# Kernel tuning notes

Measured on AMD Instinct MI355X. Metric: run time of the kernel, lower is better.

Reference implementation:

```python
import jax, jax.numpy as jnp
import numpy as np

N_NODES = 50000
N_EDGES = 600000
D = 128
BN_EPS = 1e-5


def _linear_init(key, fan_in, fan_out):
    # torch nn.Linear default: U(-1/sqrt(fan_in), 1/sqrt(fan_in)) for W and b
    kw, kb = jax.random.split(key)
    bound = 1.0 / np.sqrt(fan_in)
    W = jax.random.uniform(kw, (fan_in, fan_out), minval=-bound, maxval=bound, dtype=jnp.float32)
    b = jax.random.uniform(kb, (fan_out,), minval=-bound, maxval=bound, dtype=jnp.float32)
    return W, b


def setup_inputs() -> dict:
    key = jax.random.key(0)
    ks = jax.random.split(key, 8)
    x = jax.random.normal(ks[0], (N_NODES, D), dtype=jnp.float32)
    edge_index = jax.random.randint(ks[1], (2, N_EDGES), 0, N_NODES, dtype=jnp.int32)
    edge_attr = jax.random.normal(ks[2], (N_EDGES, D), dtype=jnp.float32)
    # MLP: [2D, D, D, D] -> Linear(2D,D)+SiLU+BN, Linear(D,D)+SiLU+BN, Linear(D,D)
    W1, b1 = _linear_init(ks[3], 2 * D, D)
    W2, b2 = _linear_init(ks[4], D, D)
    W3, b3 = _linear_init(ks[5], D, D)
    g1 = jnp.ones((D,), jnp.float32); be1 = jnp.zeros((D,), jnp.float32)
    g2 = jnp.ones((D,), jnp.float32); be2 = jnp.zeros((D,), jnp.float32)
    return {"x": x, "edge_index": edge_index, "edge_attr": edge_attr,
            "W1": W1, "b1": b1, "g1": g1, "be1": be1,
            "W2": W2, "b2": b2, "g2": g2, "be2": be2,
            "W3": W3, "b3": b3}


def _bn(h, gamma, beta):
    # BatchNorm1d in training mode: normalize with batch statistics (biased var)
    mean = jnp.mean(h, axis=0)
    var = jnp.var(h, axis=0)
    return (h - mean) * jax.lax.rsqrt(var + BN_EPS) * gamma + beta


def reference(x, edge_index, edge_attr, W1, b1, g1, be1, W2, b2, g2, be2, W3, b3):
    src = edge_index[0]
    # scatter_add over edges indexed by source node -> [N_NODES, D]
    agg = jax.ops.segment_sum(edge_attr, src, num_segments=x.shape[0])
    h = jnp.concatenate([x, agg], axis=1)  # [N, 2D]
    h = _bn(jax.nn.silu(h @ W1 + b1), g1, be1)
    h = _bn(jax.nn.silu(h @ W2 + b2), g2, be2)
    return h @ W3 + b3
```

## Files before the change

kernel.cpp:

```cpp
#include <hip/hip_runtime.h>
#include <hip/hip_bf16.h>

#define D 128

typedef __attribute__((ext_vector_type(8))) short bfrag;
typedef __attribute__((ext_vector_type(4))) float facc;
typedef __attribute__((ext_vector_type(4))) unsigned int u32x4;

__device__ __forceinline__ facc mfma16(bfrag a, bfrag b, facc c) {
    return __builtin_amdgcn_mfma_f32_16x16x32_bf16(a, b, c, 0, 0, 0);
}
__device__ __forceinline__ unsigned int bf16_rn(float f) {
    unsigned int u = __float_as_uint(f);
    u += 0x7FFF + ((u >> 16) & 1);
    return u >> 16;
}
__device__ __forceinline__ float bf16_f(unsigned int h) {
    return __uint_as_float(h << 16);
}
__device__ __forceinline__ unsigned int packf(float v) {
    unsigned int hi = bf16_rn(v);
    unsigned int lo = bf16_rn(v - bf16_f(hi));
    return (hi << 16) | lo;
}

__global__ void hist_kernel(const int* __restrict__ src,
                            int* __restrict__ counts, int nedges) {
    int e = blockIdx.x * 256 + threadIdx.x;
    if (e < nedges) atomicAdd(&counts[src[e]], 1);
}

__global__ __launch_bounds__(1024) void scan_kernel(
    const int* __restrict__ counts, int* __restrict__ off,
    int* __restrict__ cur, int n) {
    __shared__ int sdata[1024];
    const int tid = threadIdx.x;
    const int per = (n + 1023) / 1024;
    const int lo = min(tid * per, n);
    const int hi = min(lo + per, n);
    int sum = 0;
#pragma unroll 4
    for (int i = lo; i < hi; ++i) sum += counts[i];
    sdata[tid] = sum;
    __syncthreads();
#pragma unroll
    for (int d = 1; d < 1024; d <<= 1) {
        int v = (tid >= d) ? sdata[tid - d] : 0;
        __syncthreads();
        sdata[tid] += v;
        __syncthreads();
    }
    int pre = (tid == 0) ? 0 : sdata[tid - 1];
#pragma unroll 4
    for (int i = lo; i < hi; ++i) {
        off[i] = pre;
        cur[i] = pre;
        pre += counts[i];
    }
    if (tid == 0) off[n] = sdata[1023];
}

__global__ void fill_kernel(const int* __restrict__ src, int* __restrict__ cur,
                            int* __restrict__ eid, int nedges) {
    int e = blockIdx.x * 256 + threadIdx.x;
    if (e < nedges) {
        int slot = atomicAdd(&cur[src[e]], 1);
        eid[slot] = e;
    }
}

__global__ __launch_bounds__(256) void gather_kernel(
    const float* __restrict__ edge_attr, const int* __restrict__ eid,
    const int* __restrict__ off, unsigned int* __restrict__ aggp, int nnodes) {
    int node = blockIdx.x * 4 + (threadIdx.x >> 6);
    int lane = threadIdx.x & 63;
    if (node >= nnodes) return;
    int s = off[node];
    int e = off[node + 1];
    float2 acc = make_float2(0.f, 0.f);
    int i = s;
    for (; i + 8 <= e; i += 8) {
        int eb[8];
#pragma unroll
        for (int u = 0; u < 8; ++u) eb[u] = eid[i + u];
#pragma unroll
        for (int u = 0; u < 8; ++u) {
            float2 v = *((const float2*)(edge_attr + (size_t)eb[u] * D) + lane);
            acc.x += v.x;
            acc.y += v.y;
        }
    }
    for (; i < e; ++i) {
        float2 v = *((const float2*)(edge_attr + (size_t)eid[i] * D) + lane);
        acc.x += v.x;
        acc.y += v.y;
    }
    uint2 p;
    p.x = packf(acc.x);
    p.y = packf(acc.y);
    *((uint2*)(aggp + (size_t)node * D) + lane) = p;
}

__global__ void split_kernel(const float* __restrict__ x,
                             unsigned int* __restrict__ xp, int n4) {
    int i = blockIdx.x * 256 + threadIdx.x;
    if (i < n4) {
        float4 v = ((const float4*)x)[i];
        uint4 p;
        p.x = packf(v.x);
        p.y = packf(v.y);
        p.z = packf(v.z);
        p.w = packf(v.w);
        ((uint4*)xp)[i] = p;
    }
}

__global__ void prep_w_kernel(const float* __restrict__ W,
                              unsigned short* __restrict__ Wh,
                              unsigned short* __restrict__ Wl) {
    int j = blockIdx.x;
    int k = threadIdx.x;
    float w = W[(size_t)k * D + j];
    unsigned int hi = bf16_rn(w);
    size_t o = (size_t)((k >> 3) * 128 + j) * 8 + (k & 7);
    Wh[o] = (unsigned short)hi;
    Wl[o] = (unsigned short)bf16_rn(w - bf16_f(hi));
}

__global__ void fold_kernel(const float* __restrict__ sum,
                            const float* __restrict__ sq,
                            const float* __restrict__ gamma,
                            const float* __restrict__ beta,
                            const float* __restrict__ W,
                            const float* __restrict__ b,
                            unsigned short* __restrict__ Wh,
                            unsigned short* __restrict__ Wl,
                            float* __restrict__ bf, float invM) {
    int j = blockIdx.x;
    int k = threadIdx.x;
    float mean = sum[k] * invM;
    float var = sq[k] * invM - mean * mean;
    float scale = gamma[k] * rsqrtf(var + 1e-5f);
    float shift = beta[k] - mean * scale;
    float w = W[k * D + j];
    float wf = scale * w;
    unsigned int hi = bf16_rn(wf);
    size_t o = (size_t)((k >> 3) * 128 + j) * 8 + (k & 7);
    Wh[o] = (unsigned short)hi;
    Wl[o] = (unsigned short)bf16_rn(wf - bf16_f(hi));
    float v = shift * w;
#pragma unroll
    for (int of = 32; of; of >>= 1) v += __shfl_down(v, of);
    __shared__ float ws2[2];
    if ((k & 63) == 0) ws2[k >> 6] = v;
    __syncthreads();
    if (k == 0) bf[j] = b[j] + ws2[0] + ws2[1];
}

template <int K, bool SILU, bool STATS, bool PACKOUT>
__global__ __launch_bounds__(256, 2) void gemm_mfma(
    const unsigned int* __restrict__ A0, const unsigned int* __restrict__ A1,
    const unsigned short* __restrict__ Wh,
    const unsigned short* __restrict__ Wl,
    const float* __restrict__ bias, unsigned int* __restrict__ Cp,
    float* __restrict__ Cf, float* __restrict__ gsum,
    float* __restrict__ gsq, int M) {
    constexpr int NS = K / 32;
    const int tid = threadIdx.x;
    const int w = tid >> 6;
    const int l = tid & 63;
    const int lr = l & 15;
    const int lk = l >> 4;
    const int row0 = blockIdx.x * 128 + w * 32;

    facc acc[2][8];
#pragma unroll
    for (int rt = 0; rt < 2; ++rt)
#pragma unroll
        for (int ct = 0; ct < 8; ++ct)
#pragma unroll
            for (int r = 0; r < 4; ++r) acc[rt][ct][r] = 0.f;

    for (int s = 0; s < NS; ++s) {
        const int kb = s * 32 + lk * 8;
        bfrag ah[2], al[2];
#pragma unroll
        for (int rt = 0; rt < 2; ++rt) {
            const int arow = row0 + rt * 16 + lr;
            const unsigned int* As = A0;
            int kk = kb;
            if (K == 256 && s >= 4) { As = A1; kk = kb - 128; }
            u32x4 q0 = {0u, 0u, 0u, 0u}, q1 = {0u, 0u, 0u, 0u};
            if (arow < M) {
                const u32x4* p = (const u32x4*)(As + (size_t)arow * D + kk);
                q0 = p[0];
                q1 = p[1];
            }
            unsigned int ua[8] = {q0.x, q0.y, q0.z, q0.w,
                                  q1.x, q1.y, q1.z, q1.w};
            u32x4 uh, ul;
#pragma unroll
            for (int r = 0; r < 4; ++r) {
                uh[r] = __builtin_amdgcn_perm(ua[2 * r + 1], ua[2 * r],
                                              0x07060302u);
                ul[r] = __builtin_amdgcn_perm(ua[2 * r + 1], ua[2 * r],
                                              0x05040100u);
            }
            ah[rt] = __builtin_bit_cast(bfrag, uh);
            al[rt] = __builtin_bit_cast(bfrag, ul);
        }
        bfrag bh[8], bl[8];
        const int fb = (s * 4 + lk) * 128;
#pragma unroll
        for (int ct = 0; ct < 8; ++ct) {
            size_t o = (size_t)(fb + ct * 16 + lr) * 8;
            bh[ct] = *(const bfrag*)(Wh + o);
            bl[ct] = *(const bfrag*)(Wl + o);
        }
#pragma unroll
        for (int rt = 0; rt < 2; ++rt)
#pragma unroll
            for (int ct = 0; ct < 8; ++ct)
                acc[rt][ct] = mfma16(ah[rt], bh[ct], acc[rt][ct]);
#pragma unroll
        for (int rt = 0; rt < 2; ++rt)
#pragma unroll
            for (int ct = 0; ct < 8; ++ct)
                acc[rt][ct] = mfma16(ah[rt], bl[ct], acc[rt][ct]);
#pragma unroll
        for (int rt = 0; rt < 2; ++rt)
#pragma unroll
            for (int ct = 0; ct < 8; ++ct)
                acc[rt][ct] = mfma16(al[rt], bh[ct], acc[rt][ct]);
    }

    __shared__ float sred[2][4][128];
#pragma unroll
    for (int ct = 0; ct < 8; ++ct) {
        const int col = ct * 16 + lr;
        const float bj = bias[col];
        float s = 0.f, q = 0.f;
#pragma unroll
        for (int rt = 0; rt < 2; ++rt) {
            const int base = row0 + rt * 16 + lk * 4;
#pragma unroll
            for (int r = 0; r < 4; ++r) {
                int crow = base + r;
                if (crow < M) {
                    float v = acc[rt][ct][r] + bj;
                    if (SILU) v = v / (1.0f + __expf(-v));
                    if (PACKOUT) Cp[(size_t)crow * D + col] = packf(v);
                    else         Cf[(size_t)crow * D + col] = v;
                    if (STATS) { s += v; q += v * v; }
                }
            }
        }
        if (STATS) {
            s += __shfl_xor(s, 16);
            s += __shfl_xor(s, 32);
            q += __shfl_xor(q, 16);
            q += __shfl_xor(q, 32);
            if (lk == 0) {
                sred[0][w][col] = s;
                sred[1][w][col] = q;
            }
        }
    }
    if (STATS) {
        __syncthreads();
        if (tid < 128) {
            float v = sred[0][0][tid] + sred[0][1][tid] + sred[0][2][tid] +
                      sred[0][3][tid];
            unsafeAtomicAdd(&gsum[tid], v);
        } else {
            int c = tid - 128;
            float v = sred[1][0][c] + sred[1][1][c] + sred[1][2][c] +
                      sred[1][3][c];
            unsafeAtomicAdd(&gsq[c], v);
        }
    }
}

extern "C" void kernel_launch(void* const* d_in, const int* in_sizes, int n_in,
                              void* d_out, int out_size, void* d_ws,
                              size_t ws_size, hipStream_t stream) {
    const float* x     = (const float*)d_in[0];
    const int*   eidx  = (const int*)d_in[1];
    const float* eattr = (const float*)d_in[2];
    const float* W1  = (const float*)d_in[3];
    const float* b1  = (const float*)d_in[4];
    const float* g1  = (const float*)d_in[5];
    const float* be1 = (const float*)d_in[6];
    const float* W2  = (const float*)d_in[7];
    const float* b2  = (const float*)d_in[8];
    const float* g2  = (const float*)d_in[9];
    const float* be2 = (const float*)d_in[10];
    const float* W3  = (const float*)d_in[11];
    const float* b3  = (const float*)d_in[12];

    const int M = in_sizes[0] / D;
    const int E = in_sizes[1] / 2;
    const int* srcIdx = eidx;

    unsigned int* wsu = (unsigned int*)d_ws;
    unsigned int* aggp = wsu;
    unsigned int* xp   = aggp + (size_t)M * D;
    unsigned int* h1p  = xp + (size_t)M * D;
    unsigned int* h2p  = h1p + (size_t)M * D;
    float* sum1 = (float*)(h2p + (size_t)M * D);
    float* sq1  = sum1 + D;
    float* sum2 = sq1 + D;
    float* sq2  = sum2 + D;
    float* b2f  = sq2 + D;
    float* b3f  = b2f + D;
    int* counts = (int*)(b3f + D);
    int* off    = counts + M;
    int* cur    = off + M + 4;
    int* eid    = cur + M;
    unsigned short* W1h = (unsigned short*)(eid + E);
    unsigned short* W1l = W1h + 256 * D;
    unsigned short* W2h = W1l + 256 * D;
    unsigned short* W2l = W2h + D * D;
    unsigned short* W3h = W2l + D * D;
    unsigned short* W3l = W3h + D * D;

    float* out = (float*)d_out;

    hipMemsetAsync(counts, 0, (size_t)M * sizeof(int), stream);
    hipMemsetAsync(sum1, 0, 4 * D * sizeof(float), stream);

    int eblk = (E + 255) / 256;
    hist_kernel<<<eblk, 256, 0, stream>>>(srcIdx, counts, E);
    scan_kernel<<<1, 1024, 0, stream>>>(counts, off, cur, M);
    fill_kernel<<<eblk, 256, 0, stream>>>(srcIdx, cur, eid, E);
    gather_kernel<<<(M + 3) / 4, 256, 0, stream>>>(eattr, eid, off, aggp, M);

    split_kernel<<<(M * 32 + 255) / 256, 256, 0, stream>>>(x, xp, M * 32);
    prep_w_kernel<<<D, 256, 0, stream>>>(W1, W1h, W1l);

    int nblk = (M + 127) / 128;
    gemm_mfma<256, true, true, true><<<nblk, 256, 0, stream>>>(
        xp, aggp, W1h, W1l, b1, h1p, nullptr, sum1, sq1, M);
    fold_kernel<<<D, D, 0, stream>>>(sum1, sq1, g1, be1, W2, b2, W2h, W2l,
                                     b2f, 1.0f / (float)M);
    gemm_mfma<128, true, true, true><<<nblk, 256, 0, stream>>>(
        h1p, nullptr, W2h, W2l, b2f, h2p, nullptr, sum2, sq2, M);
    fold_kernel<<<D, D, 0, stream>>>(sum2, sq2, g2, be2, W3, b3, W3h, W3l,
                                     b3f, 1.0f / (float)M);
    gemm_mfma<128, false, false, false><<<nblk, 256, 0, stream>>>(
        h2p, nullptr, W3h, W3l, b3f, nullptr, out, nullptr, nullptr, M);
}
```

Before: 289.8 us.

## Merge prep kernels, parallelize prefix scan, and vectorize edge gather

Merges the histogram, x bf16 split, and W1 split kernels into one launch using block-index ranges. Replaces the single-block 1024-thread scan with a three-phase multi-block scan so the offset computation is no longer serialized on one CU. Rewrites the gather so each half-wave processes alternate edges with 16-byte nontemporal loads and combines the halves with a cross-lane shuffle. This cuts launch count and improves memory-level parallelism, at the cost of more scan launches and odd-edge handling logic.

Result: faster. 247.7 us (-14.5%).

```diff
diff --git a/kernel.cpp b/kernel.cpp
--- a/kernel.cpp
+++ b/kernel.cpp
@@ -6,6 +6,7 @@
 typedef __attribute__((ext_vector_type(8))) short bfrag;
 typedef __attribute__((ext_vector_type(4))) float facc;
 typedef __attribute__((ext_vector_type(4))) unsigned int u32x4;
+typedef __attribute__((ext_vector_type(4))) float f32x4;
 
 __device__ __forceinline__ facc mfma16(bfrag a, bfrag b, facc c) {
     return __builtin_amdgcn_mfma_f32_16x16x32_bf16(a, b, c, 0, 0, 0);
@@ -24,40 +25,104 @@
     return (hi << 16) | lo;
 }
 
-__global__ void hist_kernel(const int* __restrict__ src,
-                            int* __restrict__ counts, int nedges) {
-    int e = blockIdx.x * 256 + threadIdx.x;
-    if (e < nedges) atomicAdd(&counts[src[e]], 1);
-}
-
-__global__ __launch_bounds__(1024) void scan_kernel(
-    const int* __restrict__ counts, int* __restrict__ off,
-    int* __restrict__ cur, int n) {
-    __shared__ int sdata[1024];
+__global__ __launch_bounds__(256) void prep_kernel(
+    const int* __restrict__ src, int* __restrict__ counts, int nedges,
+    const float* __restrict__ x, unsigned int* __restrict__ xp, int n4,
+    const float* __restrict__ W1, unsigned short* __restrict__ Wh,
+    unsigned short* __restrict__ Wl, int eblk, int sblk) {
+    int b = blockIdx.x;
+    if (b < eblk) {
+        int e = b * 256 + threadIdx.x;
+        if (e < nedges) atomicAdd(&counts[src[e]], 1);
+    } else if (b < eblk + sblk) {
+        int i = (b - eblk) * 256 + threadIdx.x;
+        if (i < n4) {
+            float4 v = ((const float4*)x)[i];
+            uint4 p;
+            p.x = packf(v.x);
+            p.y = packf(v.y);
+            p.z = packf(v.z);
+            p.w = packf(v.w);
+            ((uint4*)xp)[i] = p;
+        }
+    } else {
+        int j = b - eblk - sblk;
+        int k = threadIdx.x;
+        float w = W1[(size_t)k * D + j];
+        unsigned int hi = bf16_rn(w);
+        size_t o = (size_t)((k >> 3) * 128 + j) * 8 + (k & 7);
+        Wh[o] = (unsigned short)hi;
+        Wl[o] = (unsigned short)bf16_rn(w - bf16_f(hi));
+    }
+}
+
+#define SCHUNK 2048
+__global__ __launch_bounds__(256) void scan1_kernel(
+    const int* __restrict__ counts, int* __restrict__ bsum, int n) {
+    __shared__ int sd[256];
     const int tid = threadIdx.x;
-    const int per = (n + 1023) / 1024;
-    const int lo = min(tid * per, n);
-    const int hi = min(lo + per, n);
-    int sum = 0;
-#pragma unroll 4
-    for (int i = lo; i < hi; ++i) sum += counts[i];
-    sdata[tid] = sum;
+    const int base = blockIdx.x * SCHUNK + tid * 8;
+    int s = 0;
+#pragma unroll
+    for (int j = 0; j < 8; ++j) {
+        int idx = base + j;
+        if (idx < n) s += counts[idx];
+    }
+    sd[tid] = s;
     __syncthreads();
-#pragma unroll
-    for (int d = 1; d < 1024; d <<= 1) {
-        int v = (tid >= d) ? sdata[tid - d] : 0;
+    for (int d2 = 128; d2; d2 >>= 1) {
+        if (tid < d2) sd[tid] += sd[tid + d2];
         __syncthreads();
-        sdata[tid] += v;
+    }
+    if (tid == 0) bsum[blockIdx.x] = sd[0];
+}
+__global__ void scan2_kernel(int* __restrict__ bsum, int nb) {
+    int tid = threadIdx.x;
+    int v = (tid < nb) ? bsum[tid] : 0;
+#pragma unroll
+    for (int d2 = 1; d2 < 64; d2 <<= 1) {
+        int t = __shfl_up(v, d2);
+        if (tid >= d2) v += t;
+    }
+    if (tid < nb) bsum[tid] = v;
+}
+__global__ __launch_bounds__(256) void scan3_kernel(
+    const int* __restrict__ counts, const int* __restrict__ bsum,
+    int* __restrict__ off, int* __restrict__ cur, int n) {
+    __shared__ int sd[256];
+    const int tid = threadIdx.x;
+    const int base = blockIdx.x * SCHUNK + tid * 8;
+    int loc[8];
+    int s = 0;
+#pragma unroll
+    for (int j = 0; j < 8; ++j) {
+        int idx = base + j;
+        int c = (idx < n) ? counts[idx] : 0;
+        loc[j] = c;
+        s += c;
+    }
+    sd[tid] = s;
+    __syncthreads();
+#pragma unroll
+    for (int d2 = 1; d2 < 256; d2 <<= 1) {
+        int t = (tid >= d2) ? sd[tid - d2] : 0;
         __syncthreads();
-    }
-    int pre = (tid == 0) ? 0 : sdata[tid - 1];
-#pragma unroll 4
-    for (int i = lo; i < hi; ++i) {
-        off[i] = pre;
-        cur[i] = pre;
-        pre += counts[i];
-    }
-    if (tid == 0) off[n] = sdata[1023];
+        sd[tid] += t;
+        __syncthreads();
+    }
+    int boff = (blockIdx.x == 0) ? 0 : bsum[blockIdx.x - 1];
+    int pre = boff + sd[tid] - s;
+#pragma unroll
+    for (int j = 0; j < 8; ++j) {
+        int idx = base + j;
+        if (idx < n) {
+            off[idx] = pre;
+            cur[idx] = pre;
+            pre += loc[j];
+        }
+    }
+    if (tid == 255 && base + 8 >= n && n <= blockIdx.x * SCHUNK + SCHUNK)
+        off[n] = boff + sd[255];
 }
 
 __global__ void fill_kernel(const int* __restrict__ src, int* __restrict__ cur,
@@ -75,56 +140,49 @@
     int node = blockIdx.x * 4 + (threadIdx.x >> 6);
     int lane = threadIdx.x & 63;
     if (node >= nnodes) return;
-    int s = off[node];
-    int e = off[node + 1];
-    float2 acc = make_float2(0.f, 0.f);
-    int i = s;
-    for (; i + 8 <= e; i += 8) {
-        int eb[8];
-#pragma unroll
-        for (int u = 0; u < 8; ++u) eb[u] = eid[i + u];
+    const int h = lane >> 5;
+    const int c = lane & 31;
+    int i = off[node];
+    const int e = off[node + 1];
+    f32x4 acc = {0.f, 0.f, 0.f, 0.f};
+
+    if (i < e && (i & 1)) {
+        f32x4 v = __builtin_nontemporal_load(
+            (const f32x4*)(edge_attr + (size_t)eid[i] * D) + c);
+        if (h == 0) acc += v;
+        ++i;
+    }
+    for (; i + 16 <= e; i += 16) {
+        f32x4 v[8];
 #pragma unroll
         for (int u = 0; u < 8; ++u) {
-            float2 v = *((const float2*)(edge_attr + (size_t)eb[u] * D) + lane);
-            acc.x += v.x;
-            acc.y += v.y;
-        }
-    }
-    for (; i < e; ++i) {
-        float2 v = *((const float2*)(edge_attr + (size_t)eid[i] * D) + lane);
-        acc.x += v.x;
-        acc.y += v.y;
-    }
-    uint2 p;
-    p.x = packf(acc.x);
-    p.y = packf(acc.y);
-    *((uint2*)(aggp + (size_t)node * D) + lane) = p;
-}
-
-__global__ void split_kernel(const float* __restrict__ x,
-                             unsigned int* __restrict__ xp, int n4) {
-    int i = blockIdx.x * 256 + threadIdx.x;
-    if (i < n4) {
-        float4 v = ((const float4*)x)[i];
-        uint4 p;
-        p.x = packf(v.x);
-        p.y = packf(v.y);
-        p.z = packf(v.z);
-        p.w = packf(v.w);
-        ((uint4*)xp)[i] = p;
-    }
-}
-
-__global__ void prep_w_kernel(const float* __restrict__ W,
-                              unsigned short* __restrict__ Wh,
-                              unsigned short* __restrict__ Wl) {
-    int j = blockIdx.x;
-    int k = threadIdx.x;
-    float w = W[(size_t)k * D + j];
-    unsigned int hi = bf16_rn(w);
-    size_t o = (size_t)((k >> 3) * 128 + j) * 8 + (k & 7);
-    Wh[o] = (unsigned short)hi;
-    Wl[o] = (unsigned short)bf16_rn(w - bf16_f(hi));
+            int2 ep = *(const int2*)(eid + i + 2 * u);
+            int row = h ? ep.y : ep.x;
+            v[u] = __builtin_nontemporal_load(
+                (const f32x4*)(edge_attr + (size_t)row * D) + c);
+        }
+#pragma unroll
+        for (int u = 0; u < 8; ++u) acc += v[u];
+    }
+    for (; i + 2 <= e; i += 2) {
+        int2 ep = *(const int2*)(eid + i);
+        int row = h ? ep.y : ep.x;
+        acc += __builtin_nontemporal_load(
+            (const f32x4*)(edge_attr + (size_t)row * D) + c);
+    }
+    if (i < e) {
+        f32x4 v = __builtin_nontemporal_load(
+            (const f32x4*)(edge_attr + (size_t)eid[i] * D) + c);
+        if (h == 0) acc += v;
+    }
+#pragma unroll
+    for (int r = 0; r < 4; ++r) acc[r] += __shfl_xor(acc[r], 32);
+    if (h == 0) {
+        u32x4 p;
+#pragma unroll
+        for (int r = 0; r < 4; ++r) p[r] = packf(acc[r]);
+        *((u32x4*)(aggp + (size_t)node * D) + c) = p;
+    }
 }
 
 __global__ void fold_kernel(const float* __restrict__ sum,
@@ -317,7 +375,8 @@
     int* off    = counts + M;
     int* cur    = off + M + 4;
     int* eid    = cur + M;
-    unsigned short* W1h = (unsigned short*)(eid + E);
+    int* bsum   = eid + E;
+    unsigned short* W1h = (unsigned short*)(bsum + 64);
     unsigned short* W1l = W1h + 256 * D;
     unsigned short* W2h = W1l + 256 * D;
     unsigned short* W2l = W2h + D * D;
@@ -329,14 +388,17 @@
     hipMemsetAsync(counts, 0, (size_t)M * sizeof(int), stream);
     hipMemsetAsync(sum1, 0, 4 * D * sizeof(float), stream);
 
-    int eblk = (E + 255) / 256;
-    hist_kernel<<<eblk, 256, 0, stream>>>(srcIdx, counts, E);
-    scan_kernel<<<1, 1024, 0, stream>>>(counts, off, cur, M);
+    const int eblk = (E + 255) / 256;
+    const int sblk = (M * 32 + 255) / 256;
+    prep_kernel<<<eblk + sblk + 128, 256, 0, stream>>>(
+        srcIdx, counts, E, x, xp, M * 32, W1, W1h, W1l, eblk, sblk);
+
+    const int nb = (M + SCHUNK - 1) / SCHUNK;
+    scan1_kernel<<<nb, 256, 0, stream>>>(counts, bsum, M);
+    scan2_kernel<<<1, 64, 0, stream>>>(bsum, nb);
+    scan3_kernel<<<nb, 256, 0, stream>>>(counts, bsum, off, cur, M);
     fill_kernel<<<eblk, 256, 0, stream>>>(srcIdx, cur, eid, E);
     gather_kernel<<<(M + 3) / 4, 256, 0, stream>>>(eattr, eid, off, aggp, M);
-
-    split_kernel<<<(M * 32 + 255) / 256, 256, 0, stream>>>(x, xp, M * 32);
-    prep_w_kernel<<<D, 256, 0, stream>>>(W1, W1h, W1l);
 
     int nblk = (M + 127) / 128;
     gemm_mfma<256, true, true, true><<<nblk, 256, 0, stream>>>(
```
